# Kernel tuning notes

Measured on AMD Instinct MI355X. Metric: run time of the kernel, lower is better.

## Reference

```python
import jax, jax.numpy as jnp
import numpy as np

K = 20
BN_EPS = 1e-5


def setup_inputs() -> dict:
    key = jax.random.key(0)
    ks = jax.random.split(key, 6)
    B, N, H = 2, 4096, 384
    s = lambda k, sh, sc: jax.random.normal(k, sh, dtype=jnp.float32) * sc
    return {
        "xyz": jax.random.normal(ks[0], (B, N, 3), dtype=jnp.float32),
        "W1": s(ks[1], (6, 128), 0.2),   "b1": jnp.zeros((128,), jnp.float32),
        "g1": jnp.ones((128,), jnp.float32), "be1": jnp.zeros((128,), jnp.float32),
        "W2": s(ks[2], (128, 256), 0.08), "b2": jnp.zeros((256,), jnp.float32),
        "W3": s(ks[3], (512, 512), 0.05), "b3": jnp.zeros((512,), jnp.float32),
        "g3": jnp.ones((512,), jnp.float32), "be3": jnp.zeros((512,), jnp.float32),
        "W4": s(ks[4], (512, H), 0.05),  "b4": jnp.zeros((H,), jnp.float32),
    }


def _knn_idx(x, k):
    # x: [B,N,3] -> k nearest neighbor indices (incl. self), sorted by distance
    sq = jnp.sum(x * x, axis=-1)                                  # [B,N]
    d2 = sq[:, :, None] + sq[:, None, :] - 2.0 * jnp.einsum('bnd,bmd->bnm', x, x)
    _, idx = jax.lax.top_k(-d2, k)                                # [B,N,k]
    return jax.lax.stop_gradient(idx)


def _bn_relu(h, gamma, beta):
    # BatchNorm1d in training mode: per-channel stats over (batch, length) dims.
    # h: [M, k, C]
    mu = jnp.mean(h, axis=(0, 1), keepdims=True)
    var = jnp.var(h, axis=(0, 1), keepdims=True)  # biased, matches torch BN
    return jax.nn.relu((h - mu) * jax.lax.rsqrt(var + BN_EPS) * gamma + beta)


def reference(xyz, W1, b1, g1, be1, W2, b2, W3, b3, g3, be3, W4, b4):
    B, N, _ = xyz.shape
    idx = _knn_idx(xyz, K)                                        # [B,N,K]
    nbr = jax.vmap(lambda pts, i: pts[i])(xyz, idx)               # [B,N,K,3]
    ctr = xyz[:, :, None, :]
    edge = jnp.concatenate([nbr - ctr, jnp.broadcast_to(ctr, nbr.shape)], axis=-1)
    h = edge.reshape(B * N, K, 6)                                 # [M,K,6]
    # conv1: Conv1d(6,128) -> BN -> ReLU -> Conv1d(128,256)  (kernel-1 convs == matmul)
    h = _bn_relu(h @ W1 + b1, g1, be1)
    h = h @ W2 + b2                                               # [M,K,256]
    gmax = jnp.max(h, axis=1, keepdims=True)                      # [M,1,256]
    f = jnp.concatenate([jnp.broadcast_to(gmax, h.shape), h], axis=-1)  # [M,K,512]
    # conv2: Conv1d(512,512) -> BN -> ReLU -> Conv1d(512,hidden)
    f = _bn_relu(f @ W3 + b3, g3, be3)
    f = f @ W4 + b4                                               # [M,K,H]
    feature = jnp.max(f, axis=1).reshape(B, N, -1)                # [B,N,H]
    return (xyz, feature)
```

## Files before the change

kernel.cpp:

```cpp
#include <hip/hip_runtime.h>
#include <float.h>

#define NPTS_B 4096
#define NPTS 8192
#define KNN 20
#define NSAMP (NPTS*KNN)

typedef __attribute__((ext_vector_type(8))) short bf16x8;
typedef __attribute__((ext_vector_type(4))) float f32x4;

static __device__ __forceinline__ float bf2f(unsigned short u) {
  return __uint_as_float(((unsigned int)u) << 16);
}
static __device__ __forceinline__ unsigned short f2bf(float f) {
  unsigned int u = __float_as_uint(f);
  u += 0x7fffu + ((u >> 16) & 1u);
  return (unsigned short)(u >> 16);
}
static __device__ __forceinline__ unsigned long long u64min(unsigned long long a,
                                                           unsigned long long b) {
  return a < b ? a : b;
}
static __device__ __forceinline__ unsigned long long shflx64(unsigned long long v, int m) {
  int lo = __shfl_xor((int)(unsigned int)(v & 0xffffffffull), m);
  int hi = __shfl_xor((int)(unsigned int)(v >> 32), m);
  return ((unsigned long long)(unsigned int)hi << 32) | (unsigned int)lo;
}
static __device__ __forceinline__ void gl_lds16(const void* g, void* l) {
  __builtin_amdgcn_global_load_lds(
      (const __attribute__((address_space(1))) unsigned int*)g,
      (__attribute__((address_space(3))) unsigned int*)l, 16, 0, 0);
}

__global__ __launch_bounds__(256) void wprep_kernel(const float* __restrict__ W3,
                                                    const float* __restrict__ W4,
                                                    const float* __restrict__ W2,
                                                    unsigned short* __restrict__ W3T,
                                                    unsigned short* __restrict__ W4T,
                                                    unsigned short* __restrict__ W2T) {
  int id = blockIdx.x * 256 + threadIdx.x;
  if (id < 512*512) {
    int n = id >> 9, k = id & 511;
    W3T[id] = f2bf(W3[k*512 + n]);
  } else if (id < 512*512 + 384*512) {
    int id2 = id - 512*512;
    int n = id2 >> 9, k = id2 & 511;
    W4T[id2] = f2bf(W4[k*384 + n]);
  } else {
    int id2 = id - (512*512 + 384*512);
    int n = id2 >> 7, k = id2 & 127;
    W2T[id2] = f2bf(W2[k*256 + n]);
  }
}

__global__ __launch_bounds__(256) void knn_kernel(const float* __restrict__ xyz,
                                                  int* __restrict__ idx,
                                                  float* __restrict__ out_xyz) {
#pragma clang fp contract(off)
  int p = blockIdx.x;
  int base = p & ~4095;
  int tid = threadIdx.x;
  int wv = tid >> 6;
  int ln = tid & 63;
  const float* xb = xyz + (size_t)base * 3;
  float xi0 = xyz[p*3+0], xi1 = xyz[p*3+1], xi2 = xyz[p*3+2];
  float sqi = (xi0*xi0 + xi1*xi1) + xi2*xi2;

  unsigned long long cand[16];
#pragma unroll
  for (int u = 0; u < 16; ++u) {
    int j = tid + (u << 8);
    float a0 = xb[j*3+0], a1 = xb[j*3+1], a2 = xb[j*3+2];
    float sqj = (a0*a0 + a1*a1) + a2*a2;
    float dt  = (xi0*a0 + xi1*a1) + xi2*a2;
    float d2  = (sqi + sqj) - 2.0f*dt;
    cand[u] = ((unsigned long long)__float_as_uint(d2) << 32) | (unsigned int)j;
  }
  unsigned long long myloc;
  {
    unsigned long long t[8];
#pragma unroll
    for (int u = 0; u < 8; ++u) t[u] = u64min(cand[u], cand[u + 8]);
#pragma unroll
    for (int u = 0; u < 4; ++u) t[u] = u64min(t[u], t[u + 4]);
    t[0] = u64min(t[0], t[2]); t[1] = u64min(t[1], t[3]);
    myloc = u64min(t[0], t[1]);
  }
  unsigned long long wmreg = myloc;
#pragma unroll
  for (int off = 1; off < 64; off <<= 1) wmreg = u64min(wmreg, shflx64(wmreg, off));

  __shared__ __align__(16) unsigned long long wbuf[2][4];
  __shared__ int outbuf[20];
  if (ln == 0) wbuf[0][wv] = wmreg;
  __syncthreads();

  for (int r = 0; r < 20; ++r) {
    int cur = r & 1;
    unsigned long long w0 = wbuf[cur][0], w1 = wbuf[cur][1];
    unsigned long long w2 = wbuf[cur][2], w3 = wbuf[cur][3];
    unsigned long long g = u64min(u64min(w0, w1), u64min(w2, w3));
    int wj = (int)(unsigned int)(g & 0xffffffffu);
    if (tid == (wj & 255)) {
      outbuf[r] = base + wj;
      unsigned long long m = ~0ull;
#pragma unroll
      for (int u = 0; u < 16; ++u) {
        if (cand[u] == g) cand[u] = ~0ull;
        m = u64min(m, cand[u]);
      }
      myloc = m;
    }
    if (wv == ((wj >> 6) & 3)) {
      unsigned long long t = myloc;
#pragma unroll
      for (int off = 1; off < 64; off <<= 1) t = u64min(t, shflx64(t, off));
      wmreg = t;
    }
    if (ln == 0) wbuf[cur ^ 1][wv] = wmreg;
    __syncthreads();
  }
  if (tid < 20) idx[p*20 + tid] = outbuf[tid];
  if (tid < 3) out_xyz[p*3 + tid] = xyz[p*3 + tid];
}

__global__ __launch_bounds__(256) void h1_moments_kernel(const float* __restrict__ xyz,
                                                         const int* __restrict__ idx,
                                                         float* __restrict__ mbuck) {
  int tid = threadIdx.x, blk = blockIdx.x;
  float A[33] = {};
#pragma unroll
  for (int u = 0; u < 2; ++u) {
    int s = blk*512 + (u << 8) + tid;
    unsigned int p = (unsigned int)s / 20u;
    int jg = idx[s];
    float c0 = xyz[p*3+0], c1 = xyz[p*3+1], c2 = xyz[p*3+2];
    float e[6];
    e[0] = xyz[jg*3+0] - c0; e[1] = xyz[jg*3+1] - c1; e[2] = xyz[jg*3+2] - c2;
    e[3] = c0; e[4] = c1; e[5] = c2;
    int k = 6;
#pragma unroll
    for (int d = 0; d < 6; ++d) {
      A[d] += e[d];
#pragma unroll
      for (int d2 = d; d2 < 6; ++d2) { A[k] = fmaf(e[d], e[d2], A[k]); ++k; }
    }
  }
#pragma unroll
  for (int off = 1; off < 64; off <<= 1) {
#pragma unroll
    for (int i = 0; i < 33; ++i) A[i] += __shfl_xor(A[i], off);
  }
  if ((tid & 63) == 0) {
    int b = ((blk << 2) | (tid >> 6)) & 15;
    for (int i = 0; i < 33; ++i) atomicAdd(&mbuck[b*64 + i], A[i]);
  }
}

__global__ void bn_prep1(const float* __restrict__ W1, const float* __restrict__ b1,
                         const float* __restrict__ g1, const float* __restrict__ be1,
                         const float* __restrict__ mbuck, float* __restrict__ misc) {
  __shared__ float red[33];
  int tid = threadIdx.x;
  if (tid < 33) {
    float s = 0.f;
    for (int b = 0; b < 16; ++b) s += mbuck[b*64 + tid];
    red[tid] = s;
  }
  __syncthreads();
  int c = tid;
  float w[6];
#pragma unroll
  for (int d = 0; d < 6; ++d) w[d] = W1[d*128 + c];
  const float inv = 1.0f / (float)NSAMP;
  float t = 0.f;
#pragma unroll
  for (int d = 0; d < 6; ++d) t = fmaf(w[d], red[d], t);
  t *= inv;
  float Q = 0.f;
  int k = 6;
#pragma unroll
  for (int d = 0; d < 6; ++d) {
#pragma unroll
    for (int d2 = d; d2 < 6; ++d2) {
      float coef = (d == d2) ? w[d]*w[d] : 2.f*w[d]*w[d2];
      Q = fmaf(coef, red[k], Q); ++k;
    }
  }
  Q *= inv;
  float var = Q - t*t;
  float mu = b1[c] + t;
  float a = g1[c] / sqrtf(var + 1e-5f);
  misc[c] = a;
  misc[128 + c] = be1[c] - mu*a;
}

__global__ __launch_bounds__(256) void h2_kernel(const float* __restrict__ xyz,
                                                 const int* __restrict__ idx,
                                                 const float* __restrict__ W1,
                                                 const float* __restrict__ b1,
                                                 const unsigned short* __restrict__ W2T,
                                                 const float* __restrict__ b2,
                                                 const float* __restrict__ misc,
                                                 unsigned short* __restrict__ h2out,
                                                 unsigned short* __restrict__ gmaxout) {
  int p0 = blockIdx.x << 2;
  int tid = threadIdx.x;
  int w = tid >> 6, lane = tid & 63;
  int lr = lane & 15, lg = lane >> 4;
  __shared__ float e[80][6];
  __shared__ __align__(16) unsigned short As[80][136];
  __shared__ float pool[20][264];

  bf16x8 bfr[4][4];
#pragma unroll
  for (int j = 0; j < 4; ++j)
#pragma unroll
    for (int kk = 0; kk < 4; ++kk)
      bfr[j][kk] = *(const bf16x8*)(W2T + (size_t)(w*64 + j*16 + lr)*128 + kk*32 + lg*8);

  if (tid < 80) {
    int pl = (unsigned int)tid / 20u;
    int p = p0 + pl;
    int jg = idx[p0*20 + tid];
    float xi0 = xyz[p*3+0], xi1 = xyz[p*3+1], xi2 = xyz[p*3+2];
    e[tid][0] = xyz[jg*3+0] - xi0;
    e[tid][1] = xyz[jg*3+1] - xi1;
    e[tid][2] = xyz[jg*3+2] - xi2;
    e[tid][3] = xi0; e[tid][4] = xi1; e[tid][5] = xi2;
  }
  __syncthreads();

  {
    int c = tid & 127, half = tid >> 7;
    float w1v[6];
#pragma unroll
    for (int d = 0; d < 6; ++d) w1v[d] = W1[d*128 + c];
    float b1v = b1[c], a1 = misc[c], d1 = misc[128 + c];
#pragma unroll
    for (int u = 0; u < 40; ++u) {
      int row = (u << 1) | half;
      float v = b1v;
#pragma unroll
      for (int d = 0; d < 6; ++d) v = fmaf(e[row][d], w1v[d], v);
      v = fmaxf(fmaf(a1, v, d1), 0.f);
      As[row][c] = f2bf(v);
    }
  }
  __syncthreads();

  f32x4 acc[5][4] = {};
#pragma unroll
  for (int kk = 0; kk < 4; ++kk) {
    bf16x8 a[5];
#pragma unroll
    for (int i = 0; i < 5; ++i)
      a[i] = *(const bf16x8*)&As[i*16 + lr][kk*32 + lg*8];
#pragma unroll
    for (int i = 0; i < 5; ++i)
#pragma unroll
      for (int j = 0; j < 4; ++j)
        acc[i][j] = __builtin_amdgcn_mfma_f32_16x16x32_bf16(a[i], bfr[j][kk], acc[i][j], 0, 0, 0);
  }

  float b2v[4];
#pragma unroll
  for (int j = 0; j < 4; ++j) b2v[j] = b2[w*64 + j*16 + lr];
#pragma unroll
  for (int i = 0; i < 5; ++i) {
    int rbase = p0*20 + i*16 + lg*4;
#pragma unroll
    for (int j = 0; j < 4; ++j) {
      int col = w*64 + j*16 + lr;
      float v0 = acc[i][j][0] + b2v[j];
      float v1 = acc[i][j][1] + b2v[j];
      float v2 = acc[i][j][2] + b2v[j];
      float v3 = acc[i][j][3] + b2v[j];
      h2out[(size_t)(rbase+0)*256 + col] = f2bf(v0);
      h2out[(size_t)(rbase+1)*256 + col] = f2bf(v1);
      h2out[(size_t)(rbase+2)*256 + col] = f2bf(v2);
      h2out[(size_t)(rbase+3)*256 + col] = f2bf(v3);
      pool[i*4 + lg][col] = fmaxf(fmaxf(v0, v1), fmaxf(v2, v3));
    }
  }
  __syncthreads();
#pragma unroll
  for (int l = 0; l < 4; ++l) {
    int id = tid + (l << 8);
    int q = id >> 8, col = id & 255;
    float v = pool[q*5][col];
#pragma unroll
    for (int u = 1; u < 5; ++u) v = fmaxf(v, pool[q*5 + u][col]);
    gmaxout[(size_t)(p0 + q)*256 + col] = f2bf(v);
  }
}

__global__ __launch_bounds__(512) void gemm3_kernel(const unsigned short* __restrict__ h2,
                                                    const unsigned short* __restrict__ gmax,
                                                    const unsigned short* __restrict__ W3T,
                                                    const float* __restrict__ b3,
                                                    unsigned short* __restrict__ h3,
                                                    float* __restrict__ s3buck) {
  int bid = blockIdx.x;
  int grp = bid >> 4, rem = bid & 15;
  int bn = rem >> 3;
  int bm = (grp << 3) | (rem & 7);
  int m0 = bm << 7, n0 = bn << 8;
  unsigned int pbase = (unsigned int)m0 / 20u;
  int tid = threadIdx.x;
  int lane = tid & 63, w = tid >> 6;
  int mw = w >> 2, nw = w & 3;
  int lr = lane & 15, lg = lane >> 4;
  __shared__ __align__(16) char smem[59520];
  unsigned short (*As)[64] = (unsigned short (*)[64])smem;
  unsigned short (*Bs)[64] = (unsigned short (*)[64])(smem + 16384);
  float (*Plds)[260] = (float (*)[260])(smem + 49152);
  float* ssum = (float*)(smem + 49152 + 8320);
  float* ssq  = ssum + 256;
  unsigned short (*Cs)[264] = (unsigned short (*)[264])smem;

  int rS[4], kgS[4], ksS[4];
#pragma unroll
  for (int l = 0; l < 4; ++l) {
    int id = tid + (l << 9);
    rS[l] = id >> 3;
    ksS[l] = id & 7;
    kgS[l] = ksS[l] ^ ((id >> 4) & 7);
  }
  int swz = lr >> 1;

  f32x4 accP[4] = {};
  int par = tid >> 3, paks = tid & 7;
  int pakg = paks ^ ((tid >> 4) & 7);
  for (int kc = 0; kc < 256; kc += 64) {
    if (tid < 128)
      gl_lds16(gmax + (size_t)(pbase + par)*256 + kc + (pakg << 3), &As[par][paks << 3]);
#pragma unroll
    for (int l = 0; l < 4; ++l)
      gl_lds16(W3T + (size_t)(n0 + rS[l])*512 + kc + (kgS[l] << 3), &Bs[rS[l]][ksS[l] << 3]);
    __syncthreads();
#pragma unroll
    for (int h = 0; h < 2; ++h) {
      int ch = ((h << 2) | lg) ^ swz;
      bf16x8 a = *(const bf16x8*)&As[lr][ch << 3];
#pragma unroll
      for (int j = 0; j < 4; ++j) {
        bf16x8 b = *(const bf16x8*)&Bs[nw*64 + j*16 + lr][ch << 3];
        accP[j] = __builtin_amdgcn_mfma_f32_16x16x32_bf16(a, b, accP[j], 0, 0, 0);
      }
    }
    __syncthreads();
  }
  if (mw == 0 && lg < 2) {
#pragma unroll
    for (int j = 0; j < 4; ++j)
#pragma unroll
      for (int r = 0; r < 4; ++r)
        Plds[lg*4 + r][nw*64 + j*16 + lr] = accP[j][r];
  }

  f32x4 acc[4][4] = {};
  for (int kc = 0; kc < 256; kc += 64) {
#pragma unroll
    for (int l = 0; l < 2; ++l)
      gl_lds16(h2 + (size_t)(m0 + rS[l])*256 + kc + (kgS[l] << 3), &As[rS[l]][ksS[l] << 3]);
#pragma unroll
    for (int l = 0; l < 4; ++l)
      gl_lds16(W3T + (size_t)(n0 + rS[l])*512 + (kc + 256) + (kgS[l] << 3), &Bs[rS[l]][ksS[l] << 3]);
    __syncthreads();
#pragma unroll
    for (int h = 0; h < 2; ++h) {
      int ch = ((h << 2) | lg) ^ swz;
      bf16x8 a[4], b[4];
#pragma unroll
      for (int t = 0; t < 4; ++t)
        a[t] = *(const bf16x8*)&As[mw*64 + t*16 + lr][ch << 3];
#pragma unroll
      for (int t = 0; t < 4; ++t)
        b[t] = *(const bf16x8*)&Bs[nw*64 + t*16 + lr][ch << 3];
#pragma unroll
      for (int i = 0; i < 4; ++i)
#pragma unroll
        for (int j = 0; j < 4; ++j)
          acc[i][j] = __builtin_amdgcn_mfma_f32_16x16x32_bf16(a[i], b[j], acc[i][j], 0, 0, 0);
    }
    __syncthreads();
  }

  if (tid < 256) { ssum[tid] = 0.f; ssq[tid] = 0.f; }
  __syncthreads();
  unsigned int prow[4][4];
#pragma unroll
  for (int i = 0; i < 4; ++i) {
    int rbase = m0 + mw*64 + i*16 + lg*4;
#pragma unroll
    for (int r = 0; r < 4; ++r)
      prow[i][r] = (unsigned int)(rbase + r) / 20u - pbase;
  }
#pragma unroll
  for (int half = 0; half < 2; ++half) {
    if (mw == half) {
#pragma unroll
      for (int j = 0; j < 4; ++j) {
        int colL = nw*64 + j*16 + lr;
        float b3v = b3[n0 + colL];
        float sumv = 0.f, sqv = 0.f;
#pragma unroll
        for (int i = 0; i < 4; ++i) {
#pragma unroll
          for (int r = 0; r < 4; ++r) {
            float v = acc[i][j][r] + b3v + Plds[prow[i][r]][colL];
            Cs[i*16 + lg*4 + r][colL] = f2bf(v);
            sumv += v; sqv = fmaf(v, v, sqv);
          }
        }
        sumv += __shfl_xor(sumv, 16); sumv += __shfl_xor(sumv, 32);
        sqv  += __shfl_xor(sqv, 16);  sqv  += __shfl_xor(sqv, 32);
        if (lg == 0) {
          atomicAdd(&ssum[colL], sumv);
          atomicAdd(&ssq[colL], sqv);
        }
      }
    }
    __syncthreads();
#pragma unroll
    for (int l = 0; l < 4; ++l) {
      int id = tid + (l << 9);
      int row = id >> 5, ch = id & 31;
      *(uint4*)(h3 + (size_t)(m0 + half*64 + row)*512 + n0 + (ch << 3)) =
          *(const uint4*)&Cs[row][ch << 3];
    }
    __syncthreads();
  }
  if (tid < 256) {
    int bkt = (bid & 63) * 1024;
    atomicAdd(&s3buck[bkt + n0 + tid], ssum[tid]);
    atomicAdd(&s3buck[bkt + 512 + n0 + tid], ssq[tid]);
  }
}

__global__ void bn_prep3(const float* __restrict__ g3, const float* __restrict__ be3,
                         const float* __restrict__ s3buck, float* __restrict__ misc) {
  int c = threadIdx.x;
  float s = 0.f, q = 0.f;
  for (int b = 0; b < 64; ++b) { s += s3buck[b*1024 + c]; q += s3buck[b*1024 + 512 + c]; }
  const float inv = 1.0f / (float)NSAMP;
  float mu = s * inv;
  float var = q * inv - mu * mu;
  float a = g3[c] / sqrtf(var + 1e-5f);
  misc[256 + c] = a;
  misc[768 + c] = be3[c] - mu * a;
}

__global__ __launch_bounds__(512) void gemm4_kernel(const unsigned short* __restrict__ h3,
                                                    const unsigned short* __restrict__ W4T,
                                                    const float* __restrict__ b4,
                                                    const float* __restrict__ misc,
                                                    float* __restrict__ outf) {
  int bm = blockIdx.x;
  int m0 = bm * 80;
  int tid = threadIdx.x;
  int lane = tid & 63, w = tid >> 6;
  int lr = lane & 15, lg = lane >> 4;
  __shared__ __align__(16) char smem[35072];
  unsigned short (*As)[40] = (unsigned short (*)[40])smem;
  unsigned short (*Bs)[32] = (unsigned short (*)[32])(smem + 6400);
  float (*pool)[392] = (float (*)[392])smem;
  float* af = (float*)(smem + 30976);
  float* df = af + 512;
  if (tid < 512) {
    af[tid] = misc[256 + tid];
    df[tid] = misc[768 + tid];
  }
  __syncthreads();
  f32x4 acc[5][3] = {};

  uint4 aR;
  int arow = tid >> 2, akg = tid & 3;
  if (tid < 320)
    aR = *(const uint4*)(h3 + (size_t)(m0 + arow)*512 + (akg << 3));
  int swz4 = (lr >> 1) & 3;

  for (int kc = 0; kc < 512; kc += 32) {
#pragma unroll
    for (int l = 0; l < 3; ++l) {
      int id = tid + (l << 9);
      int row = id >> 2, kgs = id & 3;
      int kg = kgs ^ ((row >> 1) & 3);
      gl_lds16(W4T + (size_t)row*512 + kc + (kg << 3), &Bs[row][kgs << 3]);
    }
    if (tid < 320) {
      int kb = kc + (akg << 3);
      unsigned int o[4];
#pragma unroll
      for (int q = 0; q < 4; ++q) {
        unsigned int u = ((const unsigned int*)&aR)[q];
        float lo = bf2f((unsigned short)(u & 0xffffu));
        float hi = bf2f((unsigned short)(u >> 16));
        int k0 = kb + q*2;
        lo = fmaxf(fmaf(af[k0],   lo, df[k0]),   0.f);
        hi = fmaxf(fmaf(af[k0+1], hi, df[k0+1]), 0.f);
        o[q] = (unsigned int)f2bf(lo) | ((unsigned int)f2bf(hi) << 16);
      }
      *(uint4*)&As[arow][akg << 3] = *(const uint4*)o;
    }
    __syncthreads();
    int kn = kc + 32;
    if (kn < 512 && tid < 320)
      aR = *(const uint4*)(h3 + (size_t)(m0 + arow)*512 + kn + (akg << 3));
    bf16x8 a[5], b[3];
#pragma unroll
    for (int t = 0; t < 5; ++t)
      a[t] = *(const bf16x8*)&As[t*16 + lr][lg << 3];
#pragma unroll
    for (int t = 0; t < 3; ++t)
      b[t] = *(const bf16x8*)&Bs[w*48 + t*16 + lr][(lg ^ swz4) << 3];
#pragma unroll
    for (int i = 0; i < 5; ++i)
#pragma unroll
      for (int j = 0; j < 3; ++j)
        acc[i][j] = __builtin_amdgcn_mfma_f32_16x16x32_bf16(a[i], b[j], acc[i][j], 0, 0, 0);
    __syncthreads();
  }

#pragma unroll
  for (int i = 0; i < 5; ++i)
#pragma unroll
    for (int j = 0; j < 3; ++j) {
      float m = fmaxf(fmaxf(acc[i][j][0], acc[i][j][1]),
                      fmaxf(acc[i][j][2], acc[i][j][3]));
      pool[i*4 + lg][w*48 + j*16 + lr] = m;
    }
  __syncthreads();
#pragma unroll
  for (int l = 0; l < 3; ++l) {
    int id = tid + (l << 9);
    int q = id / 384, c = id - q*384;
    float v = pool[q*5][c];
#pragma unroll
    for (int u = 1; u < 5; ++u) v = fmaxf(v, pool[q*5 + u][c]);
    outf[(size_t)(bm*4 + q)*384 + c] = v + b4[c];
  }
}

extern "C" void kernel_launch(void* const* d_in, const int* in_sizes, int n_in,
                              void* d_out, int out_size, void* d_ws, size_t ws_size,
                              hipStream_t stream) {
  const float* xyz = (const float*)d_in[0];
  const float* W1  = (const float*)d_in[1];
  const float* b1  = (const float*)d_in[2];
  const float* g1  = (const float*)d_in[3];
  const float* be1 = (const float*)d_in[4];
  const float* W2  = (const float*)d_in[5];
  const float* b2  = (const float*)d_in[6];
  const float* W3  = (const float*)d_in[7];
  const float* b3  = (const float*)d_in[8];
  const float* g3  = (const float*)d_in[9];
  const float* be3 = (const float*)d_in[10];
  const float* W4  = (const float*)d_in[11];
  const float* b4  = (const float*)d_in[12];

  char* ws = (char*)d_ws;
  int*            idx    = (int*)ws;
  float*          misc   = (float*)(ws + 0xA0000);
  float*          mbuck  = (float*)(ws + 0xA2000);
  float*          s3buck = (float*)(ws + 0xAA000);
  unsigned short* W3T    = (unsigned short*)(ws + 0xF0000);
  unsigned short* W4T    = (unsigned short*)(ws + 0x170000);
  unsigned short* W2T    = (unsigned short*)(ws + 0x1D0000);
  unsigned short* gmax   = (unsigned short*)(ws + 0x200000);
  unsigned short* h2     = (unsigned short*)(ws + 0x600000);
  unsigned short* h3     = (unsigned short*)(ws + 0x5600000ULL);

  float* ofp   = (float*)d_out;
  float* oxyz  = ofp;
  float* ofeat = ofp + 24576;

  hipMemsetAsync(ws + 0xA2000, 0, 0x48000, stream);

  wprep_kernel<<<(512*512 + 384*512 + 256*128)/256, 256, 0, stream>>>(W3, W4, W2, W3T, W4T, W2T);
  knn_kernel<<<NPTS, 256, 0, stream>>>(xyz, idx, oxyz);
  h1_moments_kernel<<<NSAMP/512, 256, 0, stream>>>(xyz, idx, mbuck);
  bn_prep1<<<1, 128, 0, stream>>>(W1, b1, g1, be1, mbuck, misc);
  h2_kernel<<<NPTS/4, 256, 0, stream>>>(xyz, idx, W1, b1, W2T, b2, misc, h2, gmax);
  gemm3_kernel<<<(NSAMP/128)*2, 512, 0, stream>>>(h2, gmax, W3T, b3, h3, s3buck);
  bn_prep3<<<1, 512, 0, stream>>>(g3, be3, s3buck, misc);
  gemm4_kernel<<<NPTS/4, 512, 0, stream>>>(h3, W4T, b4, misc, ofeat);
}
```

Measured before the change: 416.3 us.

## Double-buffer gemm3 K-loop with 32-wide stages and set occupancy launch bound

Restructures the gemm3 kernel's two K loops into one 16-stage software pipeline. Each stage loads a 32-wide K slice into one of two LDS buffers while MFMAs consume the other, which removes one of the two barriers per step and overlaps global-to-LDS loads with compute. It also adds a min-blocks hint of 4 to launch_bounds, which can cap registers and cause spills given the 4x4 accumulator tile. The swizzle changes to a 4-chunk XOR pattern to match the narrower rows.

Result: no change. 421.2 us (+1.2%).

```diff
diff --git a/kernel.cpp b/kernel.cpp
--- a/kernel.cpp
+++ b/kernel.cpp
@@ -295,12 +295,12 @@
   }
 }
 
-__global__ __launch_bounds__(512) void gemm3_kernel(const unsigned short* __restrict__ h2,
-                                                    const unsigned short* __restrict__ gmax,
-                                                    const unsigned short* __restrict__ W3T,
-                                                    const float* __restrict__ b3,
-                                                    unsigned short* __restrict__ h3,
-                                                    float* __restrict__ s3buck) {
+__global__ __launch_bounds__(512, 4) void gemm3_kernel(const unsigned short* __restrict__ h2,
+                                                       const unsigned short* __restrict__ gmax,
+                                                       const unsigned short* __restrict__ W3T,
+                                                       const float* __restrict__ b3,
+                                                       unsigned short* __restrict__ h3,
+                                                       float* __restrict__ s3buck) {
   int bid = blockIdx.x;
   int grp = bid >> 4, rem = bid & 15;
   int bn = rem >> 3;
@@ -312,45 +312,51 @@
   int mw = w >> 2, nw = w & 3;
   int lr = lane & 15, lg = lane >> 4;
   __shared__ __align__(16) char smem[59520];
-  unsigned short (*As)[64] = (unsigned short (*)[64])smem;
-  unsigned short (*Bs)[64] = (unsigned short (*)[64])(smem + 16384);
+  unsigned short (*As)[128][32] = (unsigned short (*)[128][32])smem;
+  unsigned short (*Bs)[256][32] = (unsigned short (*)[256][32])(smem + 16384);
   float (*Plds)[260] = (float (*)[260])(smem + 49152);
   float* ssum = (float*)(smem + 49152 + 8320);
   float* ssq  = ssum + 256;
   unsigned short (*Cs)[264] = (unsigned short (*)[264])smem;
 
-  int rS[4], kgS[4], ksS[4];
-#pragma unroll
-  for (int l = 0; l < 4; ++l) {
-    int id = tid + (l << 9);
-    rS[l] = id >> 3;
-    ksS[l] = id & 7;
-    kgS[l] = ksS[l] ^ ((id >> 4) & 7);
-  }
-  int swz = lr >> 1;
+  int arow = tid >> 2, aks = tid & 3, akg = aks ^ (arow & 3);
+
+  auto STAGE = [&](int u) {
+    int buf = u & 1;
+    int kc = (u & 7) << 5;
+    if (u < 8) {
+      if (tid < 64)
+        gl_lds16(gmax + (size_t)(pbase + arow)*256 + kc + (akg << 3),
+                 &As[buf][arow][aks << 3]);
+    } else {
+      gl_lds16(h2 + (size_t)(m0 + arow)*256 + kc + (akg << 3),
+               &As[buf][arow][aks << 3]);
+    }
+    int koff = (u < 8 ? 0 : 256) + kc;
+#pragma unroll
+    for (int l = 0; l < 2; ++l)
+      gl_lds16(W3T + (size_t)(n0 + arow + (l << 7))*512 + koff + (akg << 3),
+               &Bs[buf][arow + (l << 7)][aks << 3]);
+  };
+
+  int ch = (lg ^ (lr & 3)) << 3;
+
+  STAGE(0);
+  __syncthreads();
 
   f32x4 accP[4] = {};
-  int par = tid >> 3, paks = tid & 7;
-  int pakg = paks ^ ((tid >> 4) & 7);
-  for (int kc = 0; kc < 256; kc += 64) {
-    if (tid < 128)
-      gl_lds16(gmax + (size_t)(pbase + par)*256 + kc + (pakg << 3), &As[par][paks << 3]);
-#pragma unroll
-    for (int l = 0; l < 4; ++l)
-      gl_lds16(W3T + (size_t)(n0 + rS[l])*512 + kc + (kgS[l] << 3), &Bs[rS[l]][ksS[l] << 3]);
-    __syncthreads();
-#pragma unroll
-    for (int h = 0; h < 2; ++h) {
-      int ch = ((h << 2) | lg) ^ swz;
-      bf16x8 a = *(const bf16x8*)&As[lr][ch << 3];
-#pragma unroll
-      for (int j = 0; j < 4; ++j) {
-        bf16x8 b = *(const bf16x8*)&Bs[nw*64 + j*16 + lr][ch << 3];
-        accP[j] = __builtin_amdgcn_mfma_f32_16x16x32_bf16(a, b, accP[j], 0, 0, 0);
-      }
-    }
-    __syncthreads();
-  }
+  for (int t = 0; t < 8; ++t) {
+    STAGE(t + 1);
+    int cur = t & 1;
+    bf16x8 a = *(const bf16x8*)&As[cur][lr][ch];
+#pragma unroll
+    for (int j = 0; j < 4; ++j) {
+      bf16x8 b = *(const bf16x8*)&Bs[cur][nw*64 + j*16 + lr][ch];
+      accP[j] = __builtin_amdgcn_mfma_f32_16x16x32_bf16(a, b, accP[j], 0, 0, 0);
+    }
+    __syncthreads();
+  }
+
   if (mw == 0 && lg < 2) {
 #pragma unroll
     for (int j = 0; j < 4; ++j)
@@ -360,30 +366,21 @@
   }
 
   f32x4 acc[4][4] = {};
-  for (int kc = 0; kc < 256; kc += 64) {
-#pragma unroll
-    for (int l = 0; l < 2; ++l)
-      gl_lds16(h2 + (size_t)(m0 + rS[l])*256 + kc + (kgS[l] << 3), &As[rS[l]][ksS[l] << 3]);
-#pragma unroll
-    for (int l = 0; l < 4; ++l)
-      gl_lds16(W3T + (size_t)(n0 + rS[l])*512 + (kc + 256) + (kgS[l] << 3), &Bs[rS[l]][ksS[l] << 3]);
-    __syncthreads();
-#pragma unroll
-    for (int h = 0; h < 2; ++h) {
-      int ch = ((h << 2) | lg) ^ swz;
-      bf16x8 a[4], b[4];
-#pragma unroll
-      for (int t = 0; t < 4; ++t)
-        a[t] = *(const bf16x8*)&As[mw*64 + t*16 + lr][ch << 3];
-#pragma unroll
-      for (int t = 0; t < 4; ++t)
-        b[t] = *(const bf16x8*)&Bs[nw*64 + t*16 + lr][ch << 3];
-#pragma unroll
-      for (int i = 0; i < 4; ++i)
-#pragma unroll
-        for (int j = 0; j < 4; ++j)
-          acc[i][j] = __builtin_amdgcn_mfma_f32_16x16x32_bf16(a[i], b[j], acc[i][j], 0, 0, 0);
-    }
+  for (int t = 8; t < 16; ++t) {
+    if (t < 15) STAGE(t + 1);
+    int cur = t & 1;
+    bf16x8 a[4], b[4];
+#pragma unroll
+    for (int i = 0; i < 4; ++i)
+      a[i] = *(const bf16x8*)&As[cur][mw*64 + i*16 + lr][ch];
+#pragma unroll
+    for (int j = 0; j < 4; ++j)
+      b[j] = *(const bf16x8*)&Bs[cur][nw*64 + j*16 + lr][ch];
+#pragma unroll
+    for (int i = 0; i < 4; ++i)
+#pragma unroll
+      for (int j = 0; j < 4; ++j)
+        acc[i][j] = __builtin_amdgcn_mfma_f32_16x16x32_bf16(a[i], b[j], acc[i][j], 0, 0, 0);
     __syncthreads();
   }
 
@@ -426,9 +423,9 @@
 #pragma unroll
     for (int l = 0; l < 4; ++l) {
       int id = tid + (l << 9);
-      int row = id >> 5, ch = id & 31;
-      *(uint4*)(h3 + (size_t)(m0 + half*64 + row)*512 + n0 + (ch << 3)) =
-          *(const uint4*)&Cs[row][ch << 3];
+      int row = id >> 5, chk = id & 31;
+      *(uint4*)(h3 + (size_t)(m0 + half*64 + row)*512 + n0 + (chk << 3)) =
+          *(const uint4*)&Cs[row][chk << 3];
     }
     __syncthreads();
   }
```

## Split per-point gmax projection into separate GEMM kernel and read it from global

Applied to the files above, without the earlier changes.

The per-point gmax·W3[:256] projection was previously recomputed inside every gemm3 block, using a mostly wasted 16-row MFMA pass and an extra LDS tile. A new pgemm kernel now computes it once per point into a bf16 buffer Pg, and gemm3 adds it in the epilogue through global loads. This drops redundant MFMA work and LDS from gemm3, which also gets a launch_bounds occupancy hint of 4. In exchange there is an extra launch, gathered global reads in the epilogue, and the projection is rounded to bf16 before the add.

Measured after the change: 410.1 us. Within noise of the previous version (-1.5%).

```diff
diff --git a/kernel.cpp b/kernel.cpp
--- a/kernel.cpp
+++ b/kernel.cpp
@@ -295,31 +295,94 @@
   }
 }
 
-__global__ __launch_bounds__(512) void gemm3_kernel(const unsigned short* __restrict__ h2,
-                                                    const unsigned short* __restrict__ gmax,
+__global__ __launch_bounds__(256) void pgemm_kernel(const unsigned short* __restrict__ gmax,
                                                     const unsigned short* __restrict__ W3T,
-                                                    const float* __restrict__ b3,
-                                                    unsigned short* __restrict__ h3,
-                                                    float* __restrict__ s3buck) {
+                                                    unsigned short* __restrict__ Pg) {
+  int bid = blockIdx.x;
+  int bm = bid >> 1, bn = bid & 1;
+  int m0 = bm << 6, n0 = bn << 8;
+  int tid = threadIdx.x;
+  int lane = tid & 63, w = tid >> 6;
+  int lr = lane & 15, lg = lane >> 4;
+  __shared__ __align__(16) char smem[40960];
+  unsigned short (*As)[64] = (unsigned short (*)[64])smem;
+  unsigned short (*Bs)[64] = (unsigned short (*)[64])(smem + 8192);
+  unsigned short (*Cs)[264] = (unsigned short (*)[264])smem;
+
+  int swz = lr >> 1;
+  f32x4 acc[4][4] = {};
+  for (int kc = 0; kc < 256; kc += 64) {
+#pragma unroll
+    for (int l = 0; l < 2; ++l) {
+      int id = tid + (l << 8);
+      int row = id >> 3, ks = id & 7, kg = ks ^ ((id >> 4) & 7);
+      gl_lds16(gmax + (size_t)(m0 + row)*256 + kc + (kg << 3), &As[row][ks << 3]);
+    }
+#pragma unroll
+    for (int l = 0; l < 8; ++l) {
+      int id = tid + (l << 8);
+      int row = id >> 3, ks = id & 7, kg = ks ^ ((id >> 4) & 7);
+      gl_lds16(W3T + (size_t)(n0 + row)*512 + kc + (kg << 3), &Bs[row][ks << 3]);
+    }
+    __syncthreads();
+#pragma unroll
+    for (int h = 0; h < 2; ++h) {
+      int ch = ((h << 2) | lg) ^ swz;
+      bf16x8 a[4], b[4];
+#pragma unroll
+      for (int t = 0; t < 4; ++t)
+        a[t] = *(const bf16x8*)&As[t*16 + lr][ch << 3];
+#pragma unroll
+      for (int t = 0; t < 4; ++t)
+        b[t] = *(const bf16x8*)&Bs[w*64 + t*16 + lr][ch << 3];
+#pragma unroll
+      for (int i = 0; i < 4; ++i)
+#pragma unroll
+        for (int j = 0; j < 4; ++j)
+          acc[i][j] = __builtin_amdgcn_mfma_f32_16x16x32_bf16(a[i], b[j], acc[i][j], 0, 0, 0);
+    }
+    __syncthreads();
+  }
+#pragma unroll
+  for (int i = 0; i < 4; ++i)
+#pragma unroll
+    for (int j = 0; j < 4; ++j)
+#pragma unroll
+      for (int r = 0; r < 4; ++r)
+        Cs[i*16 + lg*4 + r][w*64 + j*16 + lr] = f2bf(acc[i][j][r]);
+  __syncthreads();
+#pragma unroll
+  for (int l = 0; l < 8; ++l) {
+    int id = tid + (l << 8);
+    int row = id >> 5, chk = id & 31;
+    *(uint4*)(Pg + (size_t)(m0 + row)*512 + n0 + (chk << 3)) =
+        *(const uint4*)&Cs[row][chk << 3];
+  }
+}
+
+__global__ __launch_bounds__(512, 4) void gemm3_kernel(const unsigned short* __restrict__ h2,
+                                                       const unsigned short* __restrict__ Pg,
+                                                       const unsigned short* __restrict__ W3T,
+                                                       const float* __restrict__ b3,
+                                                       unsigned short* __restrict__ h3,
+                                                       float* __restrict__ s3buck) {
   int bid = blockIdx.x;
   int grp = bid >> 4, rem = bid & 15;
   int bn = rem >> 3;
   int bm = (grp << 3) | (rem & 7);
   int m0 = bm << 7, n0 = bn << 8;
-  unsigned int pbase = (unsigned int)m0 / 20u;
   int tid = threadIdx.x;
   int lane = tid & 63, w = tid >> 6;
   int mw = w >> 2, nw = w & 3;
   int lr = lane & 15, lg = lane >> 4;
-  __shared__ __align__(16) char smem[59520];
+  __shared__ __align__(16) char smem[51200];
   unsigned short (*As)[64] = (unsigned short (*)[64])smem;
   unsigned short (*Bs)[64] = (unsigned short (*)[64])(smem + 16384);
-  float (*Plds)[260] = (float (*)[260])(smem + 49152);
-  float* ssum = (float*)(smem + 49152 + 8320);
+  float* ssum = (float*)(smem + 49152);
   float* ssq  = ssum + 256;
   unsigned short (*Cs)[264] = (unsigned short (*)[264])smem;
 
-  int rS[4], kgS[4], ksS[4];
+  int rS[4], ksS[4], kgS[4];
 #pragma unroll
   for (int l = 0; l < 4; ++l) {
     int id = tid + (l << 9);
@@ -329,36 +392,6 @@
   }
   int swz = lr >> 1;
 
-  f32x4 accP[4] = {};
-  int par = tid >> 3, paks = tid & 7;
-  int pakg = paks ^ ((tid >> 4) & 7);
-  for (int kc = 0; kc < 256; kc += 64) {
-    if (tid < 128)
-      gl_lds16(gmax + (size_t)(pbase + par)*256 + kc + (pakg << 3), &As[par][paks << 3]);
-#pragma unroll
-    for (int l = 0; l < 4; ++l)
-      gl_lds16(W3T + (size_t)(n0 + rS[l])*512 + kc + (kgS[l] << 3), &Bs[rS[l]][ksS[l] << 3]);
-    __syncthreads();
-#pragma unroll
-    for (int h = 0; h < 2; ++h) {
-      int ch = ((h << 2) | lg) ^ swz;
-      bf16x8 a = *(const bf16x8*)&As[lr][ch << 3];
-#pragma unroll
-      for (int j = 0; j < 4; ++j) {
-        bf16x8 b = *(const bf16x8*)&Bs[nw*64 + j*16 + lr][ch << 3];
-        accP[j] = __builtin_amdgcn_mfma_f32_16x16x32_bf16(a, b, accP[j], 0, 0, 0);
-      }
-    }
-    __syncthreads();
-  }
-  if (mw == 0 && lg < 2) {
-#pragma unroll
-    for (int j = 0; j < 4; ++j)
-#pragma unroll
-      for (int r = 0; r < 4; ++r)
-        Plds[lg*4 + r][nw*64 + j*16 + lr] = accP[j][r];
-  }
-
   f32x4 acc[4][4] = {};
   for (int kc = 0; kc < 256; kc += 64) {
 #pragma unroll
@@ -389,13 +422,13 @@
 
   if (tid < 256) { ssum[tid] = 0.f; ssq[tid] = 0.f; }
   __syncthreads();
-  unsigned int prow[4][4];
+  unsigned int pt[4][4];
 #pragma unroll
   for (int i = 0; i < 4; ++i) {
     int rbase = m0 + mw*64 + i*16 + lg*4;
 #pragma unroll
     for (int r = 0; r < 4; ++r)
-      prow[i][r] = (unsigned int)(rbase + r) / 20u - pbase;
+      pt[i][r] = (unsigned int)(rbase + r) / 20u;
   }
 #pragma unroll
   for (int half = 0; half < 2; ++half) {
@@ -409,7 +442,8 @@
         for (int i = 0; i < 4; ++i) {
 #pragma unroll
           for (int r = 0; r < 4; ++r) {
-            float v = acc[i][j][r] + b3v + Plds[prow[i][r]][colL];
+            float v = acc[i][j][r] + b3v +
+                      bf2f(Pg[(size_t)pt[i][r]*512 + n0 + colL]);
             Cs[i*16 + lg*4 + r][colL] = f2bf(v);
             sumv += v; sqv = fmaf(v, v, sqv);
           }
@@ -426,9 +460,9 @@
 #pragma unroll
     for (int l = 0; l < 4; ++l) {
       int id = tid + (l << 9);
-      int row = id >> 5, ch = id & 31;
-      *(uint4*)(h3 + (size_t)(m0 + half*64 + row)*512 + n0 + (ch << 3)) =
-          *(const uint4*)&Cs[row][ch << 3];
+      int row = id >> 5, chk = id & 31;
+      *(uint4*)(h3 + (size_t)(m0 + half*64 + row)*512 + n0 + (chk << 3)) =
+          *(const uint4*)&Cs[row][chk << 3];
     }
     __syncthreads();
   }
@@ -571,6 +605,7 @@
   unsigned short* gmax   = (unsigned short*)(ws + 0x200000);
   unsigned short* h2     = (unsigned short*)(ws + 0x600000);
   unsigned short* h3     = (unsigned short*)(ws + 0x5600000ULL);
+  unsigned short* Pg     = (unsigned short*)(ws + 0xF600000ULL);
 
   float* ofp   = (float*)d_out;
   float* oxyz  = ofp;
@@ -583,7 +618,8 @@
   h1_moments_kernel<<<NSAMP/512, 256, 0, stream>>>(xyz, idx, mbuck);
   bn_prep1<<<1, 128, 0, stream>>>(W1, b1, g1, be1, mbuck, misc);
   h2_kernel<<<NPTS/4, 256, 0, stream>>>(xyz, idx, W1, b1, W2T, b2, misc, h2, gmax);
-  gemm3_kernel<<<(NSAMP/128)*2, 512, 0, stream>>>(h2, gmax, W3T, b3, h3, s3buck);
+  pgemm_kernel<<<256, 256, 0, stream>>>(gmax, W3T, Pg);
+  gemm3_kernel<<<(NSAMP/128)*2, 512, 0, stream>>>(h2, Pg, W3T, b3, h3, s3buck);
   bn_prep3<<<1, 512, 0, stream>>>(g3, be3, s3buck, misc);
   gemm4_kernel<<<NPTS/4, 512, 0, stream>>>(h3, W4T, b4, misc, ofeat);
 }
```
